# Optimization experiments

Measured on AMD Instinct MI355X. Metric: run time of the kernel, lower is better.

The kernel has to match this reference:

```python
import jax, jax.numpy as jnp
import numpy as np

N = 50000       # nodes
E = 800000      # edges (avg degree 16)
IN_FEATS = 256
HEADS = 8
OUT_FEATS = 32
SLOPE = 0.2     # LeakyReLU negative slope


def setup_inputs() -> dict:
    key = jax.random.key(0)
    k1, k2, k3, k4, k5, k6 = jax.random.split(key, 6)
    feat = jax.random.normal(k1, (N, IN_FEATS), dtype=jnp.float32)
    # xavier-ish scaling for the linear weight, stored [in, out] for jax
    fc_w = jax.random.normal(k2, (IN_FEATS, HEADS * OUT_FEATS), dtype=jnp.float32) / np.sqrt(IN_FEATS)
    attn_l = jax.random.normal(k3, (HEADS, OUT_FEATS), dtype=jnp.float32) * 0.1
    attn_r = jax.random.normal(k4, (HEADS, OUT_FEATS), dtype=jnp.float32) * 0.1
    src = jax.random.randint(k5, (E,), 0, N, dtype=jnp.int32)
    dst = jnp.sort(jax.random.randint(k6, (E,), 0, N, dtype=jnp.int32))
    return {"feat": feat, "fc_w": fc_w, "attn_l": attn_l, "attn_r": attn_r,
            "src": src, "dst": dst}


def reference(feat, fc_w, attn_l, attn_r, src, dst):
    # dense projection: [N, H, F]
    feat_src = (feat @ fc_w).reshape(N, HEADS, OUT_FEATS)
    el = jnp.einsum('nhf,hf->nh', feat_src, attn_l)   # [N, H]
    er = jnp.einsum('nhf,hf->nh', feat_src, attn_r)   # [N, H]

    # per-edge raw score: nb.el + v.er  -> [E, H]
    e = el[src] + er[dst]
    # per-destination max over incoming edges (edge softmax stabilizer)
    m = jax.ops.segment_max(e, dst, num_segments=N)   # [N, H]
    z = e - m[dst]
    # Seastar order: exp(leaky_relu(emb - max(embs)))
    coeff = jnp.exp(jnp.where(z >= 0, z, SLOPE * z))  # [E, H]
    s = jax.ops.segment_sum(coeff, dst, num_segments=N)
    alpha = coeff / s[dst]                            # [E, H]

    # weighted scatter-sum of gathered neighbor features -> [N, H, F]
    out = jax.ops.segment_sum(alpha[:, :, None] * feat_src[src], dst, num_segments=N)
    return out
```

## Files before the change

### kernel.cpp

```cpp
#include <hip/hip_runtime.h>
#include <hip/hip_bf16.h>

#define N_NODES 50000
#define N_EDGES 800000
#define IN_F 256
#define HEADS 8
#define OUT_F 32
#define HF (HEADS * OUT_F)
#define SLOPE 0.2f

typedef __attribute__((ext_vector_type(8))) short bf16x8;
typedef __attribute__((ext_vector_type(4))) float f32x4;

__device__ __forceinline__ ushort f2bf(float f) {
  union { float f; unsigned u; } x;
  x.f = f;
  unsigned r = x.u + 0x7FFFu + ((x.u >> 16) & 1u);
  return (ushort)(r >> 16);
}

__device__ __forceinline__ float bf2f_lo(unsigned u) {
  return __uint_as_float(u << 16);
}
__device__ __forceinline__ float bf2f_hi(unsigned u) {
  return __uint_as_float(u & 0xFFFF0000u);
}

#define ROWPTR_BLOCKS ((N_NODES + 1 + 255) / 256)

__global__ __launch_bounds__(256) void prep_kernel(
    const float* __restrict__ fc_w, const float* __restrict__ attn_l,
    ushort* __restrict__ Bt, float* __restrict__ wl,
    const int* __restrict__ dst, int* __restrict__ row_ptr) {
  __shared__ float tile[32][33];
  const int b = blockIdx.x;
  const int t = threadIdx.x;

  if (b < 64) {
    const int bx = (b & 7) * 32;
    const int by = (b >> 3) * 32;
    const int tx = t & 31;
    const int ty = t >> 5;
#pragma unroll
    for (int i = 0; i < 32; i += 8)
      tile[ty + i][tx] = fc_w[(size_t)(by + ty + i) * HF + bx + tx];
    __syncthreads();
#pragma unroll
    for (int i = 0; i < 32; i += 8)
      Bt[(size_t)(bx + ty + i) * IN_F + by + tx] = f2bf(tile[tx][ty + i]);
  } else if (b == 64) {
#pragma unroll
    for (int ii = 0; ii < 8; ++ii) {
      const int idx = ii * 256 + t;
      const int k = idx >> 3;
      const int h = idx & 7;
      const float* fp = &fc_w[(size_t)k * HF + h * OUT_F];
      const float* ap = &attn_l[h * OUT_F];
      float acc = 0.f;
#pragma unroll
      for (int f = 0; f < OUT_F; f += 4) {
        float4 a = *(const float4*)&fp[f];
        float4 bb = *(const float4*)&ap[f];
        acc += a.x * bb.x + a.y * bb.y + a.z * bb.z + a.w * bb.w;
      }
      wl[idx] = acc;
    }
  } else {
    const int i = (b - 65) * 256 + t;
    if (i <= N_NODES) {
      int lo = 0, hi = N_EDGES;
      while (lo < hi) {
        int mid = (lo + hi) >> 1;
        if (dst[mid] < i) lo = mid + 1; else hi = mid;
      }
      row_ptr[i] = lo;
    }
  }
}

#define BM 64
#define BN 256
#define BK 32
#define LDA 40

__global__ __launch_bounds__(256) void gemm_mfma(
    const float* __restrict__ A, const ushort* __restrict__ Bt,
    ushort* __restrict__ Cb, int M) {
  __shared__ __align__(16) ushort As[BM * LDA];
  __shared__ __align__(16) ushort Bs[BN * LDA];

  const int t = threadIdx.x;
  const int wave = t >> 6;
  const int lane = t & 63;
  const int m0 = blockIdx.x * BM;

  const int ar = t >> 2;
  const int ak = (t & 3) * 8;
  const int br = t >> 2;
  const int bk = (t & 3) * 8;

  const int q = lane >> 4;
  const int l16 = lane & 15;
  const int wn = wave * 64;

  f32x4 acc[4][4] = {};

  for (int k0 = 0; k0 < IN_F; k0 += BK) {
    {
      float4 v0 = make_float4(0.f, 0.f, 0.f, 0.f);
      float4 v1 = make_float4(0.f, 0.f, 0.f, 0.f);
      if (m0 + ar < M) {
        const float* ap = &A[(size_t)(m0 + ar) * IN_F + k0 + ak];
        v0 = *(const float4*)ap;
        v1 = *(const float4*)(ap + 4);
      }
      union { ushort s[8]; uint4 v; } u;
      u.s[0] = f2bf(v0.x); u.s[1] = f2bf(v0.y);
      u.s[2] = f2bf(v0.z); u.s[3] = f2bf(v0.w);
      u.s[4] = f2bf(v1.x); u.s[5] = f2bf(v1.y);
      u.s[6] = f2bf(v1.z); u.s[7] = f2bf(v1.w);
      *(uint4*)&As[ar * LDA + ak] = u.v;
    }
#pragma unroll
    for (int i = 0; i < 4; ++i) {
      const int n = br + i * 64;
      *(uint4*)&Bs[n * LDA + bk] =
          *(const uint4*)&Bt[(size_t)n * IN_F + k0 + bk];
    }
    __syncthreads();

    bf16x8 aF[4], bF[4];
#pragma unroll
    for (int i = 0; i < 4; ++i)
      aF[i] = *(const bf16x8*)&As[(i * 16 + l16) * LDA + q * 8];
#pragma unroll
    for (int jj = 0; jj < 4; ++jj)
      bF[jj] = *(const bf16x8*)&Bs[(wn + jj * 16 + l16) * LDA + q * 8];
#pragma unroll
    for (int i = 0; i < 4; ++i)
#pragma unroll
      for (int jj = 0; jj < 4; ++jj)
        acc[i][jj] = __builtin_amdgcn_mfma_f32_16x16x32_bf16(
            aF[i], bF[jj], acc[i][jj], 0, 0, 0);
    __syncthreads();
  }

#pragma unroll
  for (int i = 0; i < 4; ++i) {
#pragma unroll
    for (int r = 0; r < 4; ++r) {
      const int row = m0 + 16 * i + q * 4 + r;
      if (row < M) {
#pragma unroll
        for (int jj = 0; jj < 4; ++jj) {
          const int col = wn + 16 * jj + l16;
          Cb[(size_t)row * HF + col] = f2bf(acc[i][jj][r]);
        }
      }
    }
  }
}

__global__ __launch_bounds__(256) void el_kernel(
    const float* __restrict__ feat, const float* __restrict__ wl,
    float* __restrict__ el, int NH) {
  __shared__ float wls[IN_F * HEADS];
  const int t = threadIdx.x;
#pragma unroll
  for (int i = 0; i < (IN_F * HEADS) / 256; ++i)
    wls[i * 256 + t] = wl[i * 256 + t];
  __syncthreads();

  const int idx = blockIdx.x * 256 + t;
  if (idx >= NH) return;
  const int n = idx >> 3;
  const int h = idx & 7;
  const float* fp = &feat[(size_t)n * IN_F];
  float acc = 0.f;
#pragma unroll 8
  for (int k0 = 0; k0 < IN_F; k0 += 4) {
    float4 v = *(const float4*)&fp[k0];
    acc += v.x * wls[(k0 + 0) * 8 + h] + v.y * wls[(k0 + 1) * 8 + h] +
           v.z * wls[(k0 + 2) * 8 + h] + v.w * wls[(k0 + 3) * 8 + h];
  }
  el[idx] = acc;
}

__global__ __launch_bounds__(256) void aggregate_kernel(
    const ushort* __restrict__ featb, const float* __restrict__ el,
    const int* __restrict__ src, const int* __restrict__ row_ptr,
    float* __restrict__ out) {
  const int t = threadIdx.x;
  const int wave = t >> 6;
  const int lane = t & 63;
  const int v = blockIdx.x * 4 + wave;

  const int beg = row_ptr[v];
  const int deg = row_ptr[v + 1] - beg;

  const int j = lane >> 3;
  const int h8 = lane & 7;

  float4 acc = make_float4(0.f, 0.f, 0.f, 0.f);

  if (deg == 0) {
    *(float4*)&out[(size_t)v * HF + lane * 4] = acc;
    return;
  }

  float ssum = 0.f;

  if (deg <= 64) {
    const int npass = (deg + 7) >> 3;
    int sidx[8];
    float vel[8];
    float mx = -1e30f;
#pragma unroll
    for (int p = 0; p < 8; ++p) {
      if (p < npass) {
        const int e = p * 8 + j;
        if (e < deg) {
          sidx[p] = src[beg + e];
          vel[p] = el[(size_t)sidx[p] * HEADS + h8];
        } else {
          sidx[p] = 0;
          vel[p] = -1e30f;
        }
        mx = fmaxf(mx, vel[p]);
      }
    }
    mx = fmaxf(mx, __shfl_xor(mx, 8));
    mx = fmaxf(mx, __shfl_xor(mx, 16));
    mx = fmaxf(mx, __shfl_xor(mx, 32));

#pragma unroll
    for (int p = 0; p < 8; ++p) {
      if (p < npass) {
        float cf = 0.f;
        if (p * 8 + j < deg) {
          const float z = vel[p] - mx;
          const float w = (z >= 0.f) ? z : SLOPE * z;
          cf = __expf(w);
        }
        ssum += cf;
        const int emax = min(8, deg - p * 8);
#pragma unroll
        for (int ee = 0; ee < 8; ++ee) {
          if (ee < emax) {
            const float a = __shfl(cf, ee * 8 + j);
            const int sb = __shfl(sidx[p], ee * 8);
            const uint2 u =
                *(const uint2*)&featb[(size_t)sb * HF + lane * 4];
            acc.x = fmaf(a, bf2f_lo(u.x), acc.x);
            acc.y = fmaf(a, bf2f_hi(u.x), acc.y);
            acc.z = fmaf(a, bf2f_lo(u.y), acc.z);
            acc.w = fmaf(a, bf2f_hi(u.y), acc.w);
          }
        }
      }
    }
  } else {
    float mx = -1e30f;
    for (int e = j; e < deg; e += 8)
      mx = fmaxf(mx, el[(size_t)src[beg + e] * HEADS + h8]);
    mx = fmaxf(mx, __shfl_xor(mx, 8));
    mx = fmaxf(mx, __shfl_xor(mx, 16));
    mx = fmaxf(mx, __shfl_xor(mx, 32));

    for (int p0 = 0; p0 < deg; p0 += 8) {
      float cf = 0.f;
      int sidx = 0;
      if (p0 + j < deg) {
        sidx = src[beg + p0 + j];
        const float z = el[(size_t)sidx * HEADS + h8] - mx;
        const float w = (z >= 0.f) ? z : SLOPE * z;
        cf = __expf(w);
      }
      ssum += cf;
      const int emax = min(8, deg - p0);
      for (int ee = 0; ee < emax; ++ee) {
        const float a = __shfl(cf, ee * 8 + j);
        const int sb = __shfl(sidx, ee * 8);
        const uint2 u = *(const uint2*)&featb[(size_t)sb * HF + lane * 4];
        acc.x = fmaf(a, bf2f_lo(u.x), acc.x);
        acc.y = fmaf(a, bf2f_hi(u.x), acc.y);
        acc.z = fmaf(a, bf2f_lo(u.y), acc.z);
        acc.w = fmaf(a, bf2f_hi(u.y), acc.w);
      }
    }
  }

  ssum += __shfl_xor(ssum, 8);
  ssum += __shfl_xor(ssum, 16);
  ssum += __shfl_xor(ssum, 32);
  const float inv = 1.0f / __shfl(ssum, j);
  acc.x *= inv; acc.y *= inv; acc.z *= inv; acc.w *= inv;
  *(float4*)&out[(size_t)v * HF + lane * 4] = acc;
}

extern "C" void kernel_launch(void* const* d_in, const int* in_sizes, int n_in,
                              void* d_out, int out_size, void* d_ws,
                              size_t ws_size, hipStream_t stream) {
  const float* feat = (const float*)d_in[0];
  const float* fc_w = (const float*)d_in[1];
  const float* attn_l = (const float*)d_in[2];
  const int* src = (const int*)d_in[4];
  const int* dst = (const int*)d_in[5];
  float* out = (float*)d_out;

  const int N = N_NODES;

  ushort* featb = (ushort*)d_ws;
  float* el = (float*)(featb + (size_t)N * HF);
  float* wl = el + (size_t)N * HEADS;
  ushort* Bt = (ushort*)(wl + IN_F * HEADS);
  int* row_ptr = (int*)(Bt + (size_t)IN_F * HF);

  prep_kernel<<<65 + ROWPTR_BLOCKS, 256, 0, stream>>>(fc_w, attn_l, Bt, wl,
                                                      dst, row_ptr);

  gemm_mfma<<<(N + BM - 1) / BM, 256, 0, stream>>>(feat, Bt, featb, N);

  el_kernel<<<(N * HEADS + 255) / 256, 256, 0, stream>>>(feat, wl, el,
                                                         N * HEADS);

  aggregate_kernel<<<N / 4, 256, 0, stream>>>(featb, el, src, row_ptr, out);
}
```

Measured before the change: 235.0 us.

## Make aggregation persistent per wave with software-pipelined neighbor prefetch

The aggregate kernel now launches a fixed grid of 2048 blocks, and each wave walks a contiguous range of about 7 destination nodes instead of handling exactly one. While it processes the current node, it prefetches the next node's row pointer, source indices and el scores. The eight feature gathers in each pass are batched into registers before the FMAs, so more loads are in flight at once. The fast path is narrowed to degree 32 or less, which raises register pressure and lowers wave-level parallelism in exchange for latency hiding.

```diff
diff --git a/kernel.cpp b/kernel.cpp
--- a/kernel.cpp
+++ b/kernel.cpp
@@ -186,6 +186,10 @@
   el[idx] = acc;
 }
 
+#define AGG_BLOCKS 2048
+#define AGG_WAVES (AGG_BLOCKS * 4)
+#define PER_WAVE ((N_NODES + AGG_WAVES - 1) / AGG_WAVES)
+
 __global__ __launch_bounds__(256) void aggregate_kernel(
     const ushort* __restrict__ featb, const float* __restrict__ el,
     const int* __restrict__ src, const int* __restrict__ row_ptr,
@@ -193,109 +197,149 @@
   const int t = threadIdx.x;
   const int wave = t >> 6;
   const int lane = t & 63;
-  const int v = blockIdx.x * 4 + wave;
-
-  const int beg = row_ptr[v];
-  const int deg = row_ptr[v + 1] - beg;
-
   const int j = lane >> 3;
   const int h8 = lane & 7;
-
-  float4 acc = make_float4(0.f, 0.f, 0.f, 0.f);
-
-  if (deg == 0) {
-    *(float4*)&out[(size_t)v * HF + lane * 4] = acc;
-    return;
-  }
-
-  float ssum = 0.f;
-
-  if (deg <= 64) {
+  const int wid = blockIdx.x * 4 + wave;
+
+  int v = wid * PER_WAVE;
+  const int vend = min(v + PER_WAVE, N_NODES);
+  if (v >= vend) return;
+
+  const ushort* fb_lane = featb + lane * 4;
+
+  int beg = row_ptr[v];
+  int deg = row_ptr[v + 1] - beg;
+  int sidx[4];
+  float vel[4];
+  if (deg > 0 && deg <= 32) {
     const int npass = (deg + 7) >> 3;
-    int sidx[8];
-    float vel[8];
-    float mx = -1e30f;
-#pragma unroll
-    for (int p = 0; p < 8; ++p) {
-      if (p < npass) {
-        const int e = p * 8 + j;
-        if (e < deg) {
-          sidx[p] = src[beg + e];
-          vel[p] = el[(size_t)sidx[p] * HEADS + h8];
-        } else {
-          sidx[p] = 0;
-          vel[p] = -1e30f;
+#pragma unroll
+    for (int p = 0; p < 4; ++p) {
+      sidx[p] = 0;
+      vel[p] = -1e30f;
+      if (p < npass && p * 8 + j < deg) {
+        sidx[p] = src[beg + p * 8 + j];
+        vel[p] = el[(size_t)sidx[p] * HEADS + h8];
+      }
+    }
+  }
+
+  for (; v < vend; ++v) {
+    const int vn = v + 1;
+    int beg_n = 0, deg_n = 0;
+    if (vn < vend) {
+      beg_n = row_ptr[vn];
+      deg_n = row_ptr[vn + 1] - beg_n;
+    }
+
+    float4 acc = make_float4(0.f, 0.f, 0.f, 0.f);
+    float ssum = 0.f;
+    int sidx_n[4];
+    float vel_n[4];
+    bool pfn = false;
+
+    if (deg > 0 && deg <= 32) {
+      const int npass = (deg + 7) >> 3;
+      float mx = fmaxf(fmaxf(vel[0], vel[1]), fmaxf(vel[2], vel[3]));
+      mx = fmaxf(mx, __shfl_xor(mx, 8));
+      mx = fmaxf(mx, __shfl_xor(mx, 16));
+      mx = fmaxf(mx, __shfl_xor(mx, 32));
+
+#pragma unroll
+      for (int p = 0; p < 4; ++p) {
+        if (p < npass) {
+          float cf = 0.f;
+          if (p * 8 + j < deg) {
+            const float z = vel[p] - mx;
+            const float w = (z >= 0.f) ? z : SLOPE * z;
+            cf = __expf(w);
+          }
+          ssum += cf;
+          uint2 u[8];
+#pragma unroll
+          for (int ee = 0; ee < 8; ++ee) {
+            const int sb = __shfl(sidx[p], ee * 8);
+            u[ee] = *(const uint2*)&fb_lane[(size_t)sb * HF];
+          }
+#pragma unroll
+          for (int ee = 0; ee < 8; ++ee) {
+            const float a = __shfl(cf, ee * 8 + j);
+            acc.x = fmaf(a, bf2f_lo(u[ee].x), acc.x);
+            acc.y = fmaf(a, bf2f_hi(u[ee].x), acc.y);
+            acc.z = fmaf(a, bf2f_lo(u[ee].y), acc.z);
+            acc.w = fmaf(a, bf2f_hi(u[ee].y), acc.w);
+          }
         }
-        mx = fmaxf(mx, vel[p]);
-      }
-    }
-    mx = fmaxf(mx, __shfl_xor(mx, 8));
-    mx = fmaxf(mx, __shfl_xor(mx, 16));
-    mx = fmaxf(mx, __shfl_xor(mx, 32));
-
-#pragma unroll
-    for (int p = 0; p < 8; ++p) {
-      if (p < npass) {
+      }
+    } else if (deg > 32) {
+      float mx = -1e30f;
+      for (int e = j; e < deg; e += 8)
+        mx = fmaxf(mx, el[(size_t)src[beg + e] * HEADS + h8]);
+      mx = fmaxf(mx, __shfl_xor(mx, 8));
+      mx = fmaxf(mx, __shfl_xor(mx, 16));
+      mx = fmaxf(mx, __shfl_xor(mx, 32));
+
+      for (int p0 = 0; p0 < deg; p0 += 8) {
         float cf = 0.f;
-        if (p * 8 + j < deg) {
-          const float z = vel[p] - mx;
+        int sx = 0;
+        if (p0 + j < deg) {
+          sx = src[beg + p0 + j];
+          const float z = el[(size_t)sx * HEADS + h8] - mx;
           const float w = (z >= 0.f) ? z : SLOPE * z;
           cf = __expf(w);
         }
         ssum += cf;
-        const int emax = min(8, deg - p * 8);
-#pragma unroll
-        for (int ee = 0; ee < 8; ++ee) {
-          if (ee < emax) {
-            const float a = __shfl(cf, ee * 8 + j);
-            const int sb = __shfl(sidx[p], ee * 8);
-            const uint2 u =
-                *(const uint2*)&featb[(size_t)sb * HF + lane * 4];
-            acc.x = fmaf(a, bf2f_lo(u.x), acc.x);
-            acc.y = fmaf(a, bf2f_hi(u.x), acc.y);
-            acc.z = fmaf(a, bf2f_lo(u.y), acc.z);
-            acc.w = fmaf(a, bf2f_hi(u.y), acc.w);
-          }
+        const int emax = min(8, deg - p0);
+        for (int ee = 0; ee < emax; ++ee) {
+          const float a = __shfl(cf, ee * 8 + j);
+          const int sb = __shfl(sx, ee * 8);
+          const uint2 u = *(const uint2*)&fb_lane[(size_t)sb * HF];
+          acc.x = fmaf(a, bf2f_lo(u.x), acc.x);
+          acc.y = fmaf(a, bf2f_hi(u.x), acc.y);
+          acc.z = fmaf(a, bf2f_lo(u.y), acc.z);
+          acc.w = fmaf(a, bf2f_hi(u.y), acc.w);
         }
       }
     }
-  } else {
-    float mx = -1e30f;
-    for (int e = j; e < deg; e += 8)
-      mx = fmaxf(mx, el[(size_t)src[beg + e] * HEADS + h8]);
-    mx = fmaxf(mx, __shfl_xor(mx, 8));
-    mx = fmaxf(mx, __shfl_xor(mx, 16));
-    mx = fmaxf(mx, __shfl_xor(mx, 32));
-
-    for (int p0 = 0; p0 < deg; p0 += 8) {
-      float cf = 0.f;
-      int sidx = 0;
-      if (p0 + j < deg) {
-        sidx = src[beg + p0 + j];
-        const float z = el[(size_t)sidx * HEADS + h8] - mx;
-        const float w = (z >= 0.f) ? z : SLOPE * z;
-        cf = __expf(w);
-      }
-      ssum += cf;
-      const int emax = min(8, deg - p0);
-      for (int ee = 0; ee < emax; ++ee) {
-        const float a = __shfl(cf, ee * 8 + j);
-        const int sb = __shfl(sidx, ee * 8);
-        const uint2 u = *(const uint2*)&featb[(size_t)sb * HF + lane * 4];
-        acc.x = fmaf(a, bf2f_lo(u.x), acc.x);
-        acc.y = fmaf(a, bf2f_hi(u.x), acc.y);
-        acc.z = fmaf(a, bf2f_lo(u.y), acc.z);
-        acc.w = fmaf(a, bf2f_hi(u.y), acc.w);
-      }
-    }
-  }
-
-  ssum += __shfl_xor(ssum, 8);
-  ssum += __shfl_xor(ssum, 16);
-  ssum += __shfl_xor(ssum, 32);
-  const float inv = 1.0f / __shfl(ssum, j);
-  acc.x *= inv; acc.y *= inv; acc.z *= inv; acc.w *= inv;
-  *(float4*)&out[(size_t)v * HF + lane * 4] = acc;
+
+    int npass_n = 0;
+    if (vn < vend && deg_n > 0 && deg_n <= 32) {
+      pfn = true;
+      npass_n = (deg_n + 7) >> 3;
+#pragma unroll
+      for (int p = 0; p < 4; ++p) {
+        sidx_n[p] = 0;
+        if (p < npass_n && p * 8 + j < deg_n)
+          sidx_n[p] = src[beg_n + p * 8 + j];
+      }
+    }
+
+    if (deg > 0) {
+      ssum += __shfl_xor(ssum, 8);
+      ssum += __shfl_xor(ssum, 16);
+      ssum += __shfl_xor(ssum, 32);
+      const float inv = 1.0f / __shfl(ssum, j);
+      acc.x *= inv; acc.y *= inv; acc.z *= inv; acc.w *= inv;
+    }
+    *(float4*)&out[(size_t)v * HF + lane * 4] = acc;
+
+    if (pfn) {
+#pragma unroll
+      for (int p = 0; p < 4; ++p) {
+        vel_n[p] = -1e30f;
+        if (p < npass_n && p * 8 + j < deg_n)
+          vel_n[p] = el[(size_t)sidx_n[p] * HEADS + h8];
+      }
+    }
+
+    beg = beg_n;
+    deg = (vn < vend) ? deg_n : 0;
+#pragma unroll
+    for (int p = 0; p < 4; ++p) {
+      sidx[p] = pfn ? sidx_n[p] : 0;
+      vel[p] = pfn ? vel_n[p] : -1e30f;
+    }
+  }
 }
 
 extern "C" void kernel_launch(void* const* d_in, const int* in_sizes, int n_in,
@@ -324,5 +368,6 @@
   el_kernel<<<(N * HEADS + 255) / 256, 256, 0, stream>>>(feat, wl, el,
                                                          N * HEADS);
 
-  aggregate_kernel<<<N / 4, 256, 0, stream>>>(featb, el, src, row_ptr, out);
-}
+  aggregate_kernel<<<AGG_BLOCKS, 256, 0, stream>>>(featb, el, src, row_ptr,
+                                                   out);
+}
```

Result: no change. 232.7 us (-1.0%).

## Fuse el projection into GEMM and batch neighbor feature loads in aggregation

Applied to the files above, without the earlier changes.

Folds the el computation (feat · W_l) into the MFMA GEMM kernel. It reuses the fp32 A-tile values already held in registers, reduces them across four lanes with shuffles, and drops the separate el_kernel, which re-read the whole feature matrix. The aggregation kernel now issues sixteen neighbor feature loads before consuming any of them, to increase memory-level parallelism. It also removes the per-edge emax guard by loading padded entries (sidx=0) with zero weight, which costs redundant loads for low-degree nodes and more register pressure in the GEMM.

```diff
diff --git a/kernel.cpp b/kernel.cpp
--- a/kernel.cpp
+++ b/kernel.cpp
@@ -85,9 +85,11 @@
 
 __global__ __launch_bounds__(256) void gemm_mfma(
     const float* __restrict__ A, const ushort* __restrict__ Bt,
-    ushort* __restrict__ Cb, int M) {
+    const float* __restrict__ wl, ushort* __restrict__ Cb,
+    float* __restrict__ el, int M) {
   __shared__ __align__(16) ushort As[BM * LDA];
   __shared__ __align__(16) ushort Bs[BN * LDA];
+  __shared__ __align__(16) float wls[IN_F * HEADS];
 
   const int t = threadIdx.x;
   const int wave = t >> 6;
@@ -103,12 +105,17 @@
   const int l16 = lane & 15;
   const int wn = wave * 64;
 
+#pragma unroll
+  for (int i = 0; i < (IN_F * HEADS) / 256; ++i)
+    wls[i * 256 + t] = wl[i * 256 + t];
+
   f32x4 acc[4][4] = {};
+  float ela[8] = {0.f, 0.f, 0.f, 0.f, 0.f, 0.f, 0.f, 0.f};
 
   for (int k0 = 0; k0 < IN_F; k0 += BK) {
+    float4 v0 = make_float4(0.f, 0.f, 0.f, 0.f);
+    float4 v1 = make_float4(0.f, 0.f, 0.f, 0.f);
     {
-      float4 v0 = make_float4(0.f, 0.f, 0.f, 0.f);
-      float4 v1 = make_float4(0.f, 0.f, 0.f, 0.f);
       if (m0 + ar < M) {
         const float* ap = &A[(size_t)(m0 + ar) * IN_F + k0 + ak];
         v0 = *(const float4*)ap;
@@ -129,6 +136,24 @@
     }
     __syncthreads();
 
+    {
+      const float vv[8] = {v0.x, v0.y, v0.z, v0.w, v1.x, v1.y, v1.z, v1.w};
+      const float* wrow = &wls[(k0 + ak) * HEADS];
+#pragma unroll
+      for (int kk = 0; kk < 8; ++kk) {
+        const float4 wa = *(const float4*)&wrow[kk * 8];
+        const float4 wb = *(const float4*)&wrow[kk * 8 + 4];
+        ela[0] = fmaf(vv[kk], wa.x, ela[0]);
+        ela[1] = fmaf(vv[kk], wa.y, ela[1]);
+        ela[2] = fmaf(vv[kk], wa.z, ela[2]);
+        ela[3] = fmaf(vv[kk], wa.w, ela[3]);
+        ela[4] = fmaf(vv[kk], wb.x, ela[4]);
+        ela[5] = fmaf(vv[kk], wb.y, ela[5]);
+        ela[6] = fmaf(vv[kk], wb.z, ela[6]);
+        ela[7] = fmaf(vv[kk], wb.w, ela[7]);
+      }
+    }
+
     bf16x8 aF[4], bF[4];
 #pragma unroll
     for (int i = 0; i < 4; ++i)
@@ -146,6 +171,18 @@
   }
 
 #pragma unroll
+  for (int h = 0; h < 8; ++h) {
+    ela[h] += __shfl_xor(ela[h], 1);
+    ela[h] += __shfl_xor(ela[h], 2);
+  }
+  if ((t & 3) == 0 && m0 + ar < M) {
+    *(float4*)&el[(size_t)(m0 + ar) * HEADS] =
+        make_float4(ela[0], ela[1], ela[2], ela[3]);
+    *(float4*)&el[(size_t)(m0 + ar) * HEADS + 4] =
+        make_float4(ela[4], ela[5], ela[6], ela[7]);
+  }
+
+#pragma unroll
   for (int i = 0; i < 4; ++i) {
 #pragma unroll
     for (int r = 0; r < 4; ++r) {
@@ -159,31 +196,6 @@
       }
     }
   }
-}
-
-__global__ __launch_bounds__(256) void el_kernel(
-    const float* __restrict__ feat, const float* __restrict__ wl,
-    float* __restrict__ el, int NH) {
-  __shared__ float wls[IN_F * HEADS];
-  const int t = threadIdx.x;
-#pragma unroll
-  for (int i = 0; i < (IN_F * HEADS) / 256; ++i)
-    wls[i * 256 + t] = wl[i * 256 + t];
-  __syncthreads();
-
-  const int idx = blockIdx.x * 256 + t;
-  if (idx >= NH) return;
-  const int n = idx >> 3;
-  const int h = idx & 7;
-  const float* fp = &feat[(size_t)n * IN_F];
-  float acc = 0.f;
-#pragma unroll 8
-  for (int k0 = 0; k0 < IN_F; k0 += 4) {
-    float4 v = *(const float4*)&fp[k0];
-    acc += v.x * wls[(k0 + 0) * 8 + h] + v.y * wls[(k0 + 1) * 8 + h] +
-           v.z * wls[(k0 + 2) * 8 + h] + v.w * wls[(k0 + 3) * 8 + h];
-  }
-  el[idx] = acc;
 }
 
 __global__ __launch_bounds__(256) void aggregate_kernel(
@@ -208,54 +220,73 @@
     return;
   }
 
+  const ushort* fb_lane = featb + lane * 4;
   float ssum = 0.f;
 
   if (deg <= 64) {
     const int npass = (deg + 7) >> 3;
     int sidx[8];
     float vel[8];
-    float mx = -1e30f;
 #pragma unroll
     for (int p = 0; p < 8; ++p) {
+      sidx[p] = 0;
+      vel[p] = -1e30f;
       if (p < npass) {
         const int e = p * 8 + j;
         if (e < deg) {
           sidx[p] = src[beg + e];
           vel[p] = el[(size_t)sidx[p] * HEADS + h8];
-        } else {
-          sidx[p] = 0;
-          vel[p] = -1e30f;
-        }
-        mx = fmaxf(mx, vel[p]);
-      }
-    }
+        }
+      }
+    }
+    float mx = -1e30f;
+#pragma unroll
+    for (int p = 0; p < 8; ++p) mx = fmaxf(mx, vel[p]);
     mx = fmaxf(mx, __shfl_xor(mx, 8));
     mx = fmaxf(mx, __shfl_xor(mx, 16));
     mx = fmaxf(mx, __shfl_xor(mx, 32));
 
 #pragma unroll
-    for (int p = 0; p < 8; ++p) {
-      if (p < npass) {
-        float cf = 0.f;
-        if (p * 8 + j < deg) {
-          const float z = vel[p] - mx;
+    for (int p2 = 0; p2 < 8; p2 += 2) {
+      if (p2 < npass) {
+        float cf0 = 0.f, cf1 = 0.f;
+        if (p2 * 8 + j < deg) {
+          const float z = vel[p2] - mx;
           const float w = (z >= 0.f) ? z : SLOPE * z;
-          cf = __expf(w);
-        }
-        ssum += cf;
-        const int emax = min(8, deg - p * 8);
+          cf0 = __expf(w);
+        }
+        if ((p2 + 1) * 8 + j < deg) {
+          const float z = vel[p2 + 1] - mx;
+          const float w = (z >= 0.f) ? z : SLOPE * z;
+          cf1 = __expf(w);
+        }
+        ssum += cf0 + cf1;
+        uint2 u[16];
 #pragma unroll
         for (int ee = 0; ee < 8; ++ee) {
-          if (ee < emax) {
-            const float a = __shfl(cf, ee * 8 + j);
-            const int sb = __shfl(sidx[p], ee * 8);
-            const uint2 u =
-                *(const uint2*)&featb[(size_t)sb * HF + lane * 4];
-            acc.x = fmaf(a, bf2f_lo(u.x), acc.x);
-            acc.y = fmaf(a, bf2f_hi(u.x), acc.y);
-            acc.z = fmaf(a, bf2f_lo(u.y), acc.z);
-            acc.w = fmaf(a, bf2f_hi(u.y), acc.w);
-          }
+          const int sb = __shfl(sidx[p2], ee * 8);
+          u[ee] = *(const uint2*)&fb_lane[(size_t)sb * HF];
+        }
+#pragma unroll
+        for (int ee = 0; ee < 8; ++ee) {
+          const int sb = __shfl(sidx[p2 + 1], ee * 8);
+          u[8 + ee] = *(const uint2*)&fb_lane[(size_t)sb * HF];
+        }
+#pragma unroll
+        for (int ee = 0; ee < 8; ++ee) {
+          const float a = __shfl(cf0, ee * 8 + j);
+          acc.x = fmaf(a, bf2f_lo(u[ee].x), acc.x);
+          acc.y = fmaf(a, bf2f_hi(u[ee].x), acc.y);
+          acc.z = fmaf(a, bf2f_lo(u[ee].y), acc.z);
+          acc.w = fmaf(a, bf2f_hi(u[ee].y), acc.w);
+        }
+#pragma unroll
+        for (int ee = 0; ee < 8; ++ee) {
+          const float a = __shfl(cf1, ee * 8 + j);
+          acc.x = fmaf(a, bf2f_lo(u[8 + ee].x), acc.x);
+          acc.y = fmaf(a, bf2f_hi(u[8 + ee].x), acc.y);
+          acc.z = fmaf(a, bf2f_lo(u[8 + ee].y), acc.z);
+          acc.w = fmaf(a, bf2f_hi(u[8 + ee].y), acc.w);
         }
       }
     }
@@ -269,10 +300,10 @@
 
     for (int p0 = 0; p0 < deg; p0 += 8) {
       float cf = 0.f;
-      int sidx = 0;
+      int sx = 0;
       if (p0 + j < deg) {
-        sidx = src[beg + p0 + j];
-        const float z = el[(size_t)sidx * HEADS + h8] - mx;
+        sx = src[beg + p0 + j];
+        const float z = el[(size_t)sx * HEADS + h8] - mx;
         const float w = (z >= 0.f) ? z : SLOPE * z;
         cf = __expf(w);
       }
@@ -280,8 +311,8 @@
       const int emax = min(8, deg - p0);
       for (int ee = 0; ee < emax; ++ee) {
         const float a = __shfl(cf, ee * 8 + j);
-        const int sb = __shfl(sidx, ee * 8);
-        const uint2 u = *(const uint2*)&featb[(size_t)sb * HF + lane * 4];
+        const int sb = __shfl(sx, ee * 8);
+        const uint2 u = *(const uint2*)&fb_lane[(size_t)sb * HF];
         acc.x = fmaf(a, bf2f_lo(u.x), acc.x);
         acc.y = fmaf(a, bf2f_hi(u.x), acc.y);
         acc.z = fmaf(a, bf2f_lo(u.y), acc.z);
@@ -319,10 +350,8 @@
   prep_kernel<<<65 + ROWPTR_BLOCKS, 256, 0, stream>>>(fc_w, attn_l, Bt, wl,
                                                       dst, row_ptr);
 
-  gemm_mfma<<<(N + BM - 1) / BM, 256, 0, stream>>>(feat, Bt, featb, N);
-
-  el_kernel<<<(N * HEADS + 255) / 256, 256, 0, stream>>>(feat, wl, el,
-                                                         N * HEADS);
+  gemm_mfma<<<(N + BM - 1) / BM, 256, 0, stream>>>(feat, Bt, wl, featb, el,
+                                                   N);
 
   aggregate_kernel<<<N / 4, 256, 0, stream>>>(featb, el, src, row_ptr, out);
 }
```

After: 227.4 us. -3.2%, faster.
